# Kernel tuning notes

Hardware: AMD Instinct MI355X
Metric: run time of the kernel (lower is better)

## Reference

```python
import jax, jax.numpy as jnp
import numpy as np

N = 100000      # nodes
E = 1600000     # edges (avg degree 16)
NFEAT = 128
NHID = 128
LRELU_SLOPE = 0.2

def setup_inputs() -> dict:
    key = jax.random.key(0)
    ks = jax.random.split(key, 12)
    s = 1.0 / np.sqrt(NFEAT)
    inp = {}
    inp["x"] = jax.random.normal(ks[0], (N, NFEAT), dtype=jnp.float32)
    inp["edge_row"] = jax.random.randint(ks[1], (E,), 0, N, dtype=jnp.int32)
    inp["edge_col"] = jax.random.randint(ks[2], (E,), 0, N, dtype=jnp.int32)
    inp["edge_val"] = jax.random.uniform(ks[3], (E,), dtype=jnp.float32)
    inp["norm"] = jax.random.uniform(ks[4], (N, 1), dtype=jnp.float32) * 16.0 + 1.0
    # Relation params (bias-free Linears, torch layout y = x @ W.T)
    inp["Wg1"] = jax.random.uniform(ks[5], (NFEAT, NFEAT), minval=-s, maxval=s, dtype=jnp.float32)
    inp["Wg2"] = jax.random.uniform(ks[6], (NFEAT, NFEAT), minval=-s, maxval=s, dtype=jnp.float32)
    inp["Wb1"] = jax.random.uniform(ks[7], (NFEAT, NFEAT), minval=-s, maxval=s, dtype=jnp.float32)
    inp["Wb2"] = jax.random.uniform(ks[8], (NFEAT, NFEAT), minval=-s, maxval=s, dtype=jnp.float32)
    inp["r"] = jax.random.uniform(ks[9], (1, NFEAT), minval=-s, maxval=s, dtype=jnp.float32)
    # GraphConv weight [nfeat, nhid]
    inp["gc_w"] = jax.random.uniform(ks[10], (NFEAT, NHID), minval=-s, maxval=s, dtype=jnp.float32)
    return inp

def _spmm(edge_row, edge_col, edge_val, h):
    # sparse [N,N] @ dense [N,D] via gather + segment-sum
    return jax.ops.segment_sum(edge_val[:, None] * h[edge_col], edge_row, num_segments=N)

def reference(x, edge_row, edge_col, edge_val, norm, Wg1, Wg2, Wb1, Wb2, r, gc_w):
    # neighbor = sp.mm(adj, x)
    neighbor = _spmm(edge_row, edge_col, edge_val, x)
    # Relation (ver=1, ablation=0): FiLM-modulated transE relation vector
    gamma = jax.nn.leaky_relu(x @ Wg1.T + neighbor @ Wg2.T, LRELU_SLOPE) + 1.0
    beta = jax.nn.leaky_relu(x @ Wb1.T + neighbor @ Wb2.T, LRELU_SLOPE)
    m = x + (gamma * r + beta) - neighbor
    # tail branch (head=False, ablation=0): h_s = m @ gc.weight
    h_s = m @ gc_w
    # GraphConv with adj_self = adj + I (no norm inside)
    xw = x @ gc_w
    h_k = _spmm(edge_row, edge_col, edge_val, xw) + xw
    h_k = (h_k + h_s) / (norm + 1.0)
    return (h_k, m)
```

## Files before the change

### kernel.cpp

```cpp
#include <hip/hip_runtime.h>

#define N_NODES 100000
#define NFEAT 128
#define E_EDGES 1600000
#define LRELU_SLOPE 0.2f
#define BM 32
#define NBUCK 196
#define BROWS 512
#define BCAP 12288
#define CB_BLOCKS 256
#define CB_PER 6250
#define XB_BLOCKS 3125
#define PK_BLOCKS 320

typedef short bf16x8 __attribute__((ext_vector_type(8)));
typedef float f32x4 __attribute__((ext_vector_type(4)));

__device__ __forceinline__ ushort f2bf(float f) {
    union { float f; uint u; } v; v.f = f;
    uint u = v.u;
    return (ushort)((u + 0x7fffu + ((u >> 16) & 1u)) >> 16);
}
__device__ __forceinline__ float bf2f(ushort s) {
    union { uint u; float f; } v; v.u = ((uint)s) << 16;
    return v.f;
}
__device__ __forceinline__ float blo(uint u) {
    union { uint u; float f; } v; v.u = u << 16; return v.f;
}
__device__ __forceinline__ float bhi(uint u) {
    union { uint u; float f; } v; v.u = u & 0xFFFF0000u; return v.f;
}

__global__ __launch_bounds__(256) void mega_prep(
    const int* __restrict__ er, const int* __restrict__ ec,
    const float* __restrict__ ev, int* __restrict__ cursorB,
    int2* __restrict__ stg,
    const float* __restrict__ x, ushort* __restrict__ xb,
    const float* __restrict__ Wg1, const float* __restrict__ Wg2,
    const float* __restrict__ Wb1, const float* __restrict__ Wb2,
    const float* __restrict__ gcw,
    ushort* __restrict__ W1p, ushort* __restrict__ W2p)
{
    __shared__ int hist[NBUCK];
    __shared__ int cbase[NBUCK];
    const int bid = blockIdx.x;
    const int tid = threadIdx.x;

    if (bid < CB_BLOCKS) {
        int e0 = bid * CB_PER, e1 = e0 + CB_PER;
        if (tid < NBUCK) hist[tid] = 0;
        __syncthreads();
        for (int e = e0 + tid; e < e1; e += 256) atomicAdd(&hist[er[e] >> 9], 1);
        __syncthreads();
        if (tid < NBUCK) {
            int h = hist[tid];
            cbase[tid] = (h > 0) ? (tid * BCAP + atomicAdd(&cursorB[tid], h)) : 0;
            hist[tid] = 0;
        }
        __syncthreads();
        for (int e = e0 + tid; e < e1; e += 256) {
            int r = er[e];
            int bkt = r >> 9;
            int loc = atomicAdd(&hist[bkt], 1);
            int2 o;
            o.x = (ec[e] << 9) | (r & (BROWS - 1));
            o.y = __float_as_int(ev[e]);
            stg[cbase[bkt] + loc] = o;
        }
    } else if (bid < CB_BLOCKS + XB_BLOCKS) {
        size_t base = ((size_t)(bid - CB_BLOCKS) * 256 + tid) * 16;
        float4 a = *reinterpret_cast<const float4*>(x + base);
        float4 b = *reinterpret_cast<const float4*>(x + base + 4);
        float4 c = *reinterpret_cast<const float4*>(x + base + 8);
        float4 d = *reinterpret_cast<const float4*>(x + base + 12);
        uint4 o1, o2;
        o1.x = (uint)f2bf(a.x) | ((uint)f2bf(a.y) << 16);
        o1.y = (uint)f2bf(a.z) | ((uint)f2bf(a.w) << 16);
        o1.z = (uint)f2bf(b.x) | ((uint)f2bf(b.y) << 16);
        o1.w = (uint)f2bf(b.z) | ((uint)f2bf(b.w) << 16);
        o2.x = (uint)f2bf(c.x) | ((uint)f2bf(c.y) << 16);
        o2.y = (uint)f2bf(c.z) | ((uint)f2bf(c.w) << 16);
        o2.z = (uint)f2bf(d.x) | ((uint)f2bf(d.y) << 16);
        o2.w = (uint)f2bf(d.z) | ((uint)f2bf(d.w) << 16);
        *reinterpret_cast<uint4*>(xb + base) = o1;
        *reinterpret_cast<uint4*>(xb + base + 8) = o2;
    } else {
        int idx = (bid - CB_BLOCKS - XB_BLOCKS) * 256 + tid;
        if (idx < 65536) {
            int jj = idx & 7;
            int lane = (idx >> 3) & 63;
            int tile = idx >> 9;
            int nt = tile & 15, kt = tile >> 4;
            int k = kt * 32 + (lane >> 4) * 8 + jj;
            int j = nt * 16 + (lane & 15);
            float v;
            if (j < 128) v = (k < 128) ? Wg1[j * 128 + k] : Wg2[j * 128 + (k - 128)];
            else { int c = j - 128; v = (k < 128) ? Wb1[c * 128 + k] : Wb2[c * 128 + (k - 128)]; }
            W1p[idx] = f2bf(v);
        } else if (idx < 81920) {
            int i2 = idx - 65536;
            int jj = i2 & 7;
            int lane = (i2 >> 3) & 63;
            int tile = i2 >> 9;
            int nt = tile & 7, kt = tile >> 3;
            int k = kt * 32 + (lane >> 4) * 8 + jj;
            int j = nt * 16 + (lane & 15);
            W2p[i2] = f2bf(gcw[k * 128 + j]);
        }
    }
}

__global__ __launch_bounds__(512) void build196(
    const int* __restrict__ cursorB, const int2* __restrict__ stg,
    int2* __restrict__ csr_cv, int* __restrict__ rowstart,
    int* __restrict__ cnt)
{
    __shared__ int rowhist[BROWS];
    __shared__ int cur[BROWS];
    __shared__ int tsum[512];
    const int b = blockIdx.x;
    const int tid = threadIdx.x;

    tsum[tid] = (tid < NBUCK) ? cursorB[tid] : 0;
    __syncthreads();
    for (int off = 1; off < 512; off <<= 1) {
        int v = (tid >= off) ? tsum[tid - off] : 0;
        __syncthreads();
        tsum[tid] += v;
        __syncthreads();
    }
    const int cntE = cursorB[b];
    const int base = tsum[b] - cntE;
    const int baseIn = b * BCAP;
    __syncthreads();

    rowhist[tid] = 0;
    __syncthreads();
    for (int i = tid; i < cntE; i += 512)
        atomicAdd(&rowhist[stg[baseIn + i].x & (BROWS - 1)], 1);
    __syncthreads();
    int a = rowhist[tid];
    tsum[tid] = a;
    __syncthreads();
    for (int off = 1; off < 512; off <<= 1) {
        int v = (tid >= off) ? tsum[tid - off] : 0;
        __syncthreads();
        tsum[tid] += v;
        __syncthreads();
    }
    int ex = tsum[tid] - a;
    int row = b * BROWS + tid;
    if (row < N_NODES) {
        rowstart[row] = base + ex;
        cnt[row] = a;
    }
    cur[tid] = ex;
    __syncthreads();
    for (int i = tid; i < cntE; i += 512) {
        int2 e = stg[baseIn + i];
        int rl = e.x & (BROWS - 1);
        int loc = atomicAdd(&cur[rl], 1);
        int2 o; o.x = (e.x >> 9) << 8; o.y = e.y;
        csr_cv[base + loc] = o;
    }
}

__global__ __launch_bounds__(512, 8) void fused_all(
    const int* __restrict__ rowstart, const int* __restrict__ cnt,
    const int2* __restrict__ csr_cv, const ushort* __restrict__ xb,
    const float* __restrict__ norm, const float* __restrict__ rvec,
    const ushort* __restrict__ W1p, const ushort* __restrict__ W2p,
    float* __restrict__ hk, float* __restrict__ mout)
{
    __shared__ ushort SM[16384];
    char* asb = (char*)SM;
    char* gbb = (char*)(SM + 8192);

    const int tid = threadIdx.x;
    const int lane = tid & 63;
    const int w = tid >> 6;
    const int g = lane >> 4;
    const int s = lane & 15;
    const int node0 = blockIdx.x * BM;

    {
        int rr = tid >> 4;
        int cq = tid & 15;
        uint4 v = *reinterpret_cast<const uint4*>(xb + (size_t)(node0 + rr) * 128 + cq * 8);
        *(uint4*)(asb + ((rr * 512 + cq * 16) ^ ((rr & 7) << 4))) = v;
    }

    const char* xbase = (const char*)xb + s * 16;
#pragma unroll 1
    for (int i = 0; i < 4; i++) {
        int rr = w * 4 + i;
        int row = node0 + rr;
        const int2* cv = csr_cv + rowstart[row];
        int deg = cnt[row];
        float ac0 = 0.f, ac1 = 0.f, ac2 = 0.f, ac3 = 0.f;
        float ac4 = 0.f, ac5 = 0.f, ac6 = 0.f, ac7 = 0.f;
#pragma unroll 1
        for (int j = 0; j < deg; j += 8) {
            int i0 = j + g;
            int i1 = j + 4 + g;
            int c0 = (i0 < deg) ? i0 : deg - 1;
            int c1 = (i1 < deg) ? i1 : deg - 1;
            int2 e0 = cv[c0];
            int2 e1 = cv[c1];
            uint4 v0 = *reinterpret_cast<const uint4*>(xbase + e0.x);
            uint4 v1 = *reinterpret_cast<const uint4*>(xbase + e1.x);
            float f0 = (i0 < deg) ? __int_as_float(e0.y) : 0.f;
            float f1 = (i1 < deg) ? __int_as_float(e1.y) : 0.f;
            ac0 += f0 * blo(v0.x); ac1 += f0 * bhi(v0.x);
            ac2 += f0 * blo(v0.y); ac3 += f0 * bhi(v0.y);
            ac4 += f0 * blo(v0.z); ac5 += f0 * bhi(v0.z);
            ac6 += f0 * blo(v0.w); ac7 += f0 * bhi(v0.w);
            ac0 += f1 * blo(v1.x); ac1 += f1 * bhi(v1.x);
            ac2 += f1 * blo(v1.y); ac3 += f1 * bhi(v1.y);
            ac4 += f1 * blo(v1.z); ac5 += f1 * bhi(v1.z);
            ac6 += f1 * blo(v1.w); ac7 += f1 * bhi(v1.w);
        }
        ac0 += __shfl_xor(ac0, 16, 64); ac0 += __shfl_xor(ac0, 32, 64);
        ac1 += __shfl_xor(ac1, 16, 64); ac1 += __shfl_xor(ac1, 32, 64);
        ac2 += __shfl_xor(ac2, 16, 64); ac2 += __shfl_xor(ac2, 32, 64);
        ac3 += __shfl_xor(ac3, 16, 64); ac3 += __shfl_xor(ac3, 32, 64);
        ac4 += __shfl_xor(ac4, 16, 64); ac4 += __shfl_xor(ac4, 32, 64);
        ac5 += __shfl_xor(ac5, 16, 64); ac5 += __shfl_xor(ac5, 32, 64);
        ac6 += __shfl_xor(ac6, 16, 64); ac6 += __shfl_xor(ac6, 32, 64);
        ac7 += __shfl_xor(ac7, 16, 64); ac7 += __shfl_xor(ac7, 32, 64);
        if (g == 0) {
            uint4 o;
            o.x = (uint)f2bf(ac0) | ((uint)f2bf(ac1) << 16);
            o.y = (uint)f2bf(ac2) | ((uint)f2bf(ac3) << 16);
            o.z = (uint)f2bf(ac4) | ((uint)f2bf(ac5) << 16);
            o.w = (uint)f2bf(ac6) | ((uint)f2bf(ac7) << 16);
            *(uint4*)(asb + ((rr * 512 + 256 + s * 16) ^ ((rr & 7) << 4))) = o;
        }
    }
    __syncthreads();

    f32x4 acc[2][2];
#pragma unroll
    for (int mt = 0; mt < 2; mt++)
#pragma unroll
        for (int nl = 0; nl < 2; nl++) acc[mt][nl] = (f32x4){0.f, 0.f, 0.f, 0.f};

#pragma unroll
    for (int kt = 0; kt < 8; kt++) {
        bf16x8 af[2];
#pragma unroll
        for (int mt = 0; mt < 2; mt++) {
            int row = mt * 16 + (lane & 15);
            int off = (row * 512 + kt * 64 + (lane >> 4) * 16) ^ ((row & 7) << 4);
            af[mt] = *(bf16x8*)(asb + off);
        }
#pragma unroll
        for (int nl = 0; nl < 2; nl++) {
            int nt = w * 2 + nl;
            bf16x8 bfg = *(const bf16x8*)(W1p + (((kt * 16 + nt) * 64 + lane) << 3));
#pragma unroll
            for (int mt = 0; mt < 2; mt++)
                acc[mt][nl] = __builtin_amdgcn_mfma_f32_16x16x32_bf16(af[mt], bfg, acc[mt][nl], 0, 0, 0);
        }
    }

#pragma unroll
    for (int mt = 0; mt < 2; mt++)
#pragma unroll
        for (int nl = 0; nl < 2; nl++) {
            int j = (w * 2 + nl) * 16 + (lane & 15);
#pragma unroll
            for (int reg = 0; reg < 4; reg++) {
                int row = mt * 16 + (lane >> 4) * 4 + reg;
                int off = (row * 512 + j * 2) ^ ((row & 7) << 4);
                *(ushort*)(gbb + off) = f2bf(acc[mt][nl][reg]);
            }
        }
    __syncthreads();

    {
        int c = tid & 127;
        float rv = rvec[c];
        int rg = tid >> 7;
#pragma unroll 4
        for (int i = 0; i < 8; i++) {
            int row = rg * 8 + i;
            int swz = (row & 7) << 4;
            int bx = (row * 512 + c * 2) ^ swz;
            int bn = (row * 512 + 256 + c * 2) ^ swz;
            float graw = bf2f(*(ushort*)(gbb + bx));
            float braw = bf2f(*(ushort*)(gbb + bn));
            float xv = bf2f(*(ushort*)(asb + bx));
            float nv = bf2f(*(ushort*)(asb + bn));
            float gamma = ((graw > 0.f) ? graw : LRELU_SLOPE * graw) + 1.f;
            float beta = (braw > 0.f) ? braw : LRELU_SLOPE * braw;
            float gb_ = gamma * rv + beta;
            float mv = xv + gb_ - nv;
            float tv = 2.f * xv + gb_;
            mout[(size_t)(node0 + row) * 128 + c] = mv;
            *(ushort*)(asb + bx) = f2bf(tv);
        }
    }
    __syncthreads();

    f32x4 acc2[2];
#pragma unroll
    for (int mt = 0; mt < 2; mt++) acc2[mt] = (f32x4){0.f, 0.f, 0.f, 0.f};

#pragma unroll
    for (int kt = 0; kt < 4; kt++) {
        bf16x8 af[2];
#pragma unroll
        for (int mt = 0; mt < 2; mt++) {
            int row = mt * 16 + (lane & 15);
            int off = (row * 512 + kt * 64 + (lane >> 4) * 16) ^ ((row & 7) << 4);
            af[mt] = *(bf16x8*)(asb + off);
        }
        bf16x8 bfg = *(const bf16x8*)(W2p + (((kt * 8 + w) * 64 + lane) << 3));
#pragma unroll
        for (int mt = 0; mt < 2; mt++)
            acc2[mt] = __builtin_amdgcn_mfma_f32_16x16x32_bf16(af[mt], bfg, acc2[mt], 0, 0, 0);
    }

#pragma unroll
    for (int mt = 0; mt < 2; mt++) {
        int col = w * 16 + (lane & 15);
#pragma unroll
        for (int reg = 0; reg < 4; reg++) {
            int row = mt * 16 + (lane >> 4) * 4 + reg;
            int node = node0 + row;
            float inv = 1.f / (norm[node] + 1.f);
            hk[(size_t)node * 128 + col] = acc2[mt][reg] * inv;
        }
    }
}

extern "C" void kernel_launch(void* const* d_in, const int* in_sizes, int n_in,
                              void* d_out, int out_size, void* d_ws, size_t ws_size,
                              hipStream_t stream)
{
    const float* x    = (const float*)d_in[0];
    const int*   er   = (const int*)d_in[1];
    const int*   ec   = (const int*)d_in[2];
    const float* ev   = (const float*)d_in[3];
    const float* norm = (const float*)d_in[4];
    const float* Wg1  = (const float*)d_in[5];
    const float* Wg2  = (const float*)d_in[6];
    const float* Wb1  = (const float*)d_in[7];
    const float* Wb2  = (const float*)d_in[8];
    const float* r    = (const float*)d_in[9];
    const float* gcw  = (const float*)d_in[10];

    float* out  = (float*)d_out;
    float* hk   = out;
    float* mout = out + (size_t)N_NODES * NFEAT;

    ushort* xb       = (ushort*)d_ws;
    int2*   csr_cv   = (int2*)(xb + (size_t)N_NODES * NFEAT);
    ushort* W1p      = (ushort*)(csr_cv + E_EDGES);
    ushort* W2p      = W1p + 65536;
    int*    cnt      = (int*)(W2p + 16384);
    int*    rowstart = cnt + N_NODES;
    int*    cursorB  = rowstart + N_NODES;

    int2* stg = (int2*)hk;

    hipMemsetAsync(cursorB, 0, NBUCK * sizeof(int), stream);

    mega_prep<<<CB_BLOCKS + XB_BLOCKS + PK_BLOCKS, 256, 0, stream>>>(
        er, ec, ev, cursorB, stg, x, xb,
        Wg1, Wg2, Wb1, Wb2, gcw, W1p, W2p);

    build196<<<NBUCK, 512, 0, stream>>>(cursorB, stg, csr_cv, rowstart, cnt);

    fused_all<<<N_NODES / BM, 512, 0, stream>>>(
        rowstart, cnt, csr_cv, xb, norm, r, W1p, W2p, hk, mout);
}
```

Before: 161.7 us.

## Bucket edges per 32-node tile and sort in-block, dropping CSR build kernel

Edges are now scattered directly into one bucket per 32-row tile of the fused kernel, with each bucket capped at 2048 edges. The fused kernel loads its bucket, counting-sorts it by row into shared memory and pads each row to a multiple of 8, so the SpMM loop needs no bounds checks. This removes the separate CSR build kernel, the global CSR array and the rowstart/cnt arrays, saving one launch and one pass over the edges. In exchange, the fixed per-tile capacity (2048 edges, up to 1024 read per block) could overflow under skewed degree distributions. The per-tile scatter also uses 3125 shared-memory counters per block instead of 196.

Result: no change. 163.0 us (+0.8%).

```diff
diff --git a/kernel.cpp b/kernel.cpp
--- a/kernel.cpp
+++ b/kernel.cpp
@@ -5,11 +5,10 @@
 #define E_EDGES 1600000
 #define LRELU_SLOPE 0.2f
 #define BM 32
-#define NBUCK 196
-#define BROWS 512
-#define BCAP 12288
-#define CB_BLOCKS 256
-#define CB_PER 6250
+#define NB2 3125
+#define SCAP 2048
+#define SC_BLOCKS 128
+#define SC_PER 12500
 #define XB_BLOCKS 3125
 #define PK_BLOCKS 320
 
@@ -42,34 +41,31 @@
     const float* __restrict__ gcw,
     ushort* __restrict__ W1p, ushort* __restrict__ W2p)
 {
-    __shared__ int hist[NBUCK];
-    __shared__ int cbase[NBUCK];
+    __shared__ int harr[NB2];
     const int bid = blockIdx.x;
     const int tid = threadIdx.x;
 
-    if (bid < CB_BLOCKS) {
-        int e0 = bid * CB_PER, e1 = e0 + CB_PER;
-        if (tid < NBUCK) hist[tid] = 0;
+    if (bid < SC_BLOCKS) {
+        const int e0 = bid * SC_PER, e1 = e0 + SC_PER;
+        for (int k = tid; k < NB2; k += 256) harr[k] = 0;
         __syncthreads();
-        for (int e = e0 + tid; e < e1; e += 256) atomicAdd(&hist[er[e] >> 9], 1);
+        for (int e = e0 + tid; e < e1; e += 256) atomicAdd(&harr[er[e] >> 5], 1);
         __syncthreads();
-        if (tid < NBUCK) {
-            int h = hist[tid];
-            cbase[tid] = (h > 0) ? (tid * BCAP + atomicAdd(&cursorB[tid], h)) : 0;
-            hist[tid] = 0;
+        for (int k = tid; k < NB2; k += 256) {
+            int h = harr[k];
+            if (h) harr[k] = (k * SCAP + atomicAdd(&cursorB[k], h)) << 8;
         }
         __syncthreads();
         for (int e = e0 + tid; e < e1; e += 256) {
             int r = er[e];
-            int bkt = r >> 9;
-            int loc = atomicAdd(&hist[bkt], 1);
+            int t = atomicAdd(&harr[r >> 5], 1);
             int2 o;
-            o.x = (ec[e] << 9) | (r & (BROWS - 1));
+            o.x = (ec[e] << 13) | (r & 31);
             o.y = __float_as_int(ev[e]);
-            stg[cbase[bkt] + loc] = o;
-        }
-    } else if (bid < CB_BLOCKS + XB_BLOCKS) {
-        size_t base = ((size_t)(bid - CB_BLOCKS) * 256 + tid) * 16;
+            stg[(t >> 8) + (t & 255)] = o;
+        }
+    } else if (bid < SC_BLOCKS + XB_BLOCKS) {
+        size_t base = ((size_t)(bid - SC_BLOCKS) * 256 + tid) * 16;
         float4 a = *reinterpret_cast<const float4*>(x + base);
         float4 b = *reinterpret_cast<const float4*>(x + base + 4);
         float4 c = *reinterpret_cast<const float4*>(x + base + 8);
@@ -86,7 +82,7 @@
         *reinterpret_cast<uint4*>(xb + base) = o1;
         *reinterpret_cast<uint4*>(xb + base + 8) = o2;
     } else {
-        int idx = (bid - CB_BLOCKS - XB_BLOCKS) * 256 + tid;
+        int idx = (bid - SC_BLOCKS - XB_BLOCKS) * 256 + tid;
         if (idx < 65536) {
             int jj = idx & 7;
             int lane = (idx >> 3) & 63;
@@ -111,78 +107,26 @@
     }
 }
 
-__global__ __launch_bounds__(512) void build196(
-    const int* __restrict__ cursorB, const int2* __restrict__ stg,
-    int2* __restrict__ csr_cv, int* __restrict__ rowstart,
-    int* __restrict__ cnt)
-{
-    __shared__ int rowhist[BROWS];
-    __shared__ int cur[BROWS];
-    __shared__ int tsum[512];
-    const int b = blockIdx.x;
-    const int tid = threadIdx.x;
-
-    tsum[tid] = (tid < NBUCK) ? cursorB[tid] : 0;
-    __syncthreads();
-    for (int off = 1; off < 512; off <<= 1) {
-        int v = (tid >= off) ? tsum[tid - off] : 0;
-        __syncthreads();
-        tsum[tid] += v;
-        __syncthreads();
-    }
-    const int cntE = cursorB[b];
-    const int base = tsum[b] - cntE;
-    const int baseIn = b * BCAP;
-    __syncthreads();
-
-    rowhist[tid] = 0;
-    __syncthreads();
-    for (int i = tid; i < cntE; i += 512)
-        atomicAdd(&rowhist[stg[baseIn + i].x & (BROWS - 1)], 1);
-    __syncthreads();
-    int a = rowhist[tid];
-    tsum[tid] = a;
-    __syncthreads();
-    for (int off = 1; off < 512; off <<= 1) {
-        int v = (tid >= off) ? tsum[tid - off] : 0;
-        __syncthreads();
-        tsum[tid] += v;
-        __syncthreads();
-    }
-    int ex = tsum[tid] - a;
-    int row = b * BROWS + tid;
-    if (row < N_NODES) {
-        rowstart[row] = base + ex;
-        cnt[row] = a;
-    }
-    cur[tid] = ex;
-    __syncthreads();
-    for (int i = tid; i < cntE; i += 512) {
-        int2 e = stg[baseIn + i];
-        int rl = e.x & (BROWS - 1);
-        int loc = atomicAdd(&cur[rl], 1);
-        int2 o; o.x = (e.x >> 9) << 8; o.y = e.y;
-        csr_cv[base + loc] = o;
-    }
-}
-
 __global__ __launch_bounds__(512, 8) void fused_all(
-    const int* __restrict__ rowstart, const int* __restrict__ cnt,
-    const int2* __restrict__ csr_cv, const ushort* __restrict__ xb,
+    const int* __restrict__ cursorB, const int2* stg,
+    const ushort* __restrict__ xb,
     const float* __restrict__ norm, const float* __restrict__ rvec,
     const ushort* __restrict__ W1p, const ushort* __restrict__ W2p,
-    float* __restrict__ hk, float* __restrict__ mout)
+    float* hk, float* __restrict__ mout)
 {
     __shared__ ushort SM[16384];
+    __shared__ int h32[32], rs32[32], pd32[32], cur32[32];
     char* asb = (char*)SM;
     char* gbb = (char*)(SM + 8192);
+    int2* elist = (int2*)gbb;
 
     const int tid = threadIdx.x;
     const int lane = tid & 63;
     const int w = tid >> 6;
     const int g = lane >> 4;
     const int s = lane & 15;
-    const int node0 = blockIdx.x * BM;
+    const int b = blockIdx.x;
+    const int node0 = b * BM;
 
     {
         int rr = tid >> 4;
@@ -191,35 +135,60 @@
         *(uint4*)(asb + ((rr * 512 + cq * 16) ^ ((rr & 7) << 4))) = v;
     }
 
+    const int cntE = cursorB[b];
+    const int2* sb = stg + (size_t)b * SCAP;
+    int2 E0, E1;
+    const bool v0 = tid < cntE, v1 = tid + 512 < cntE;
+    if (v0) E0 = sb[tid];
+    if (v1) E1 = sb[tid + 512];
+    if (tid < 32) h32[tid] = 0;
+    __syncthreads();
+    if (v0) atomicAdd(&h32[E0.x & 31], 1);
+    if (v1) atomicAdd(&h32[E1.x & 31], 1);
+    __syncthreads();
+    if (tid < 64) {
+        int pc = 0;
+        if (tid < 32) { int h = h32[tid]; pc = (h + 7) & ~7; cur32[tid] = 0; }
+        int v = pc;
+        for (int off = 1; off < 32; off <<= 1) {
+            int t = __shfl_up(v, off, 64);
+            if (lane >= off) v += t;
+        }
+        if (tid < 32) { rs32[tid] = v - pc; pd32[tid] = pc; }
+    }
+    __syncthreads();
+    if (v0) { int rl = E0.x & 31; elist[rs32[rl] + atomicAdd(&cur32[rl], 1)] = E0; }
+    if (v1) { int rl = E1.x & 31; elist[rs32[rl] + atomicAdd(&cur32[rl], 1)] = E1; }
+    if (tid < 32) {
+        int rs = rs32[tid];
+        for (int j = h32[tid]; j < pd32[tid]; ++j) elist[rs + j] = make_int2(tid, 0);
+    }
+    __syncthreads();
+
     const char* xbase = (const char*)xb + s * 16;
 #pragma unroll 1
     for (int i = 0; i < 4; i++) {
         int rr = w * 4 + i;
-        int row = node0 + rr;
-        const int2* cv = csr_cv + rowstart[row];
-        int deg = cnt[row];
+        const int2* el = elist + rs32[rr];
+        int pd = pd32[rr];
         float ac0 = 0.f, ac1 = 0.f, ac2 = 0.f, ac3 = 0.f;
         float ac4 = 0.f, ac5 = 0.f, ac6 = 0.f, ac7 = 0.f;
-#pragma unroll 1
-        for (int j = 0; j < deg; j += 8) {
-            int i0 = j + g;
-            int i1 = j + 4 + g;
-            int c0 = (i0 < deg) ? i0 : deg - 1;
-            int c1 = (i1 < deg) ? i1 : deg - 1;
-            int2 e0 = cv[c0];
-            int2 e1 = cv[c1];
-            uint4 v0 = *reinterpret_cast<const uint4*>(xbase + e0.x);
-            uint4 v1 = *reinterpret_cast<const uint4*>(xbase + e1.x);
-            float f0 = (i0 < deg) ? __int_as_float(e0.y) : 0.f;
-            float f1 = (i1 < deg) ? __int_as_float(e1.y) : 0.f;
-            ac0 += f0 * blo(v0.x); ac1 += f0 * bhi(v0.x);
-            ac2 += f0 * blo(v0.y); ac3 += f0 * bhi(v0.y);
-            ac4 += f0 * blo(v0.z); ac5 += f0 * bhi(v0.z);
-            ac6 += f0 * blo(v0.w); ac7 += f0 * bhi(v0.w);
-            ac0 += f1 * blo(v1.x); ac1 += f1 * bhi(v1.x);
-            ac2 += f1 * blo(v1.y); ac3 += f1 * bhi(v1.y);
-            ac4 += f1 * blo(v1.z); ac5 += f1 * bhi(v1.z);
-            ac6 += f1 * blo(v1.w); ac7 += f1 * bhi(v1.w);
+#pragma unroll 2
+        for (int j = 0; j < pd; j += 8) {
+            int2 e0 = el[j + g];
+            int2 e1 = el[j + 4 + g];
+            uint4 q0 = *reinterpret_cast<const uint4*>(xbase + (e0.x >> 5));
+            uint4 q1 = *reinterpret_cast<const uint4*>(xbase + (e1.x >> 5));
+            float f0 = __int_as_float(e0.y);
+            float f1 = __int_as_float(e1.y);
+            ac0 += f0 * blo(q0.x); ac1 += f0 * bhi(q0.x);
+            ac2 += f0 * blo(q0.y); ac3 += f0 * bhi(q0.y);
+            ac4 += f0 * blo(q0.z); ac5 += f0 * bhi(q0.z);
+            ac6 += f0 * blo(q0.w); ac7 += f0 * bhi(q0.w);
+            ac0 += f1 * blo(q1.x); ac1 += f1 * bhi(q1.x);
+            ac2 += f1 * blo(q1.y); ac3 += f1 * bhi(q1.y);
+            ac4 += f1 * blo(q1.z); ac5 += f1 * bhi(q1.z);
+            ac6 += f1 * blo(q1.w); ac7 += f1 * bhi(q1.w);
         }
         ac0 += __shfl_xor(ac0, 16, 64); ac0 += __shfl_xor(ac0, 32, 64);
         ac1 += __shfl_xor(ac1, 16, 64); ac1 += __shfl_xor(ac1, 32, 64);
@@ -356,24 +325,19 @@
     float* hk   = out;
     float* mout = out + (size_t)N_NODES * NFEAT;
 
-    ushort* xb       = (ushort*)d_ws;
-    int2*   csr_cv   = (int2*)(xb + (size_t)N_NODES * NFEAT);
-    ushort* W1p      = (ushort*)(csr_cv + E_EDGES);
-    ushort* W2p      = W1p + 65536;
-    int*    cnt      = (int*)(W2p + 16384);
-    int*    rowstart = cnt + N_NODES;
-    int*    cursorB  = rowstart + N_NODES;
+    ushort* xb      = (ushort*)d_ws;
+    ushort* W1p     = xb + (size_t)N_NODES * NFEAT;
+    ushort* W2p     = W1p + 65536;
+    int*    cursorB = (int*)(W2p + 16384);
 
     int2* stg = (int2*)hk;
 
-    hipMemsetAsync(cursorB, 0, NBUCK * sizeof(int), stream);
-
-    mega_prep<<<CB_BLOCKS + XB_BLOCKS + PK_BLOCKS, 256, 0, stream>>>(
+    hipMemsetAsync(cursorB, 0, NB2 * sizeof(int), stream);
+
+    mega_prep<<<SC_BLOCKS + XB_BLOCKS + PK_BLOCKS, 256, 0, stream>>>(
         er, ec, ev, cursorB, stg, x, xb,
         Wg1, Wg2, Wb1, Wb2, gcw, W1p, W2p);
 
-    build196<<<NBUCK, 512, 0, stream>>>(cursorB, stg, csr_cv, rowstart, cnt);
-
-    fused_all<<<N_NODES / BM, 512, 0, stream>>>(
-        rowstart, cnt, csr_cv, xb, norm, r, W1p, W2p, hk, mout);
-}
+    fused_all<<<NB2, 512, 0, stream>>>(
+        cursorB, stg, xb, norm, r, W1p, W2p, hk, mout);
+}
```
